# Kernel tuning notes

Measured on AMD Instinct MI355X. Metric: run time of the kernel, lower is better.

The kernel has to match this reference:

```python
import jax, jax.numpy as jnp
import numpy as np
import math

NH, DH, BS, LOCAL, RAND, NCLS = 12, 64, 49, 3, 3, 1
WINDOW = (8, 14, 14)
NKV = LOCAL + RAND


def make_rel_pos_index():
    ws = WINDOW
    rel_size = [2 * w - 1 for w in ws]
    coords = np.stack(np.meshgrid(*[np.arange(w) for w in ws], indexing='ij')).reshape(len(ws), -1)
    rel = (coords[:, :, None] - coords[:, None, :]).transpose(1, 2, 0).astype(np.int64)
    for i, w in enumerate(ws):
        rel[:, :, i] += w - 1
    for i, r in enumerate(rel_size[1:]):
        rel[:, :, :i + 1] *= r
    n = coords.shape[1]
    S = n + NCLS
    idx = np.zeros((S, S), dtype=np.int64)
    idx[NCLS:, NCLS:] = rel.sum(-1)
    start = int(np.prod(rel_size))
    idx[:NCLS, NCLS:] = np.arange(NCLS)[:, None] + start
    start += NCLS
    idx[NCLS:, :NCLS] = np.arange(NCLS)[None, :] + start
    start += NCLS
    idx[:NCLS, :NCLS] = np.arange(NCLS ** 2).reshape(NCLS, NCLS) + start
    return idx.astype(np.int32)


def setup_inputs() -> dict:
    key = jax.random.key(0)
    ks = jax.random.split(key, 8)
    B, S, D = 8, 1569, 768
    M = (S - NCLS) // BS  # 32 blocks
    hidden_states = jax.random.normal(ks[0], (B, S, D), dtype=jnp.float32)
    Wq = jax.random.normal(ks[1], (D, D), dtype=jnp.float32) * 0.02
    bq = jax.random.normal(ks[2], (D,), dtype=jnp.float32) * 0.02
    Wk = jax.random.normal(ks[3], (D, D), dtype=jnp.float32) * 0.02
    Wv = jax.random.normal(ks[4], (D, D), dtype=jnp.float32) * 0.02
    bv = jax.random.normal(ks[5], (D,), dtype=jnp.float32) * 0.02
    rel_table = jax.random.normal(ks[6], (10938, NH), dtype=jnp.float32) * 0.02
    rel_pos_index = jnp.asarray(make_rel_pos_index())
    rand_idx = jnp.sort(jax.random.randint(ks[7], (M, RAND), 0, M), axis=1).astype(jnp.int32)
    return {"hidden_states": hidden_states, "Wq": Wq, "bq": bq, "Wk": Wk, "Wv": Wv,
            "bv": bv, "rel_table": rel_table, "rel_pos_index": rel_pos_index, "rand_idx": rand_idx}


def reference(hidden_states, Wq, bq, Wk, Wv, bv, rel_table, rel_pos_index, rand_idx):
    B, S, D = hidden_states.shape
    scale = 1.0 / math.sqrt(DH)
    q = hidden_states @ Wq + bq
    k = hidden_states @ Wk          # key has no bias in BeitSelfAttention
    v = hidden_states @ Wv + bv
    split = lambda x: x.reshape(B, S, NH, DH).transpose(0, 2, 1, 3)  # b h s d
    q, k, v = split(q), split(k), split(v)

    # --- dense attention for cls queries over all keys ---
    cls_q = q[:, :, :NCLS]
    sim_cls = jnp.einsum('bhid,bhjd->bhij', cls_q, k) * scale
    bias_cls = rel_table[rel_pos_index[:NCLS, :]]           # [ncls, S, H]
    sim_cls = sim_cls + bias_cls.transpose(2, 0, 1)[None]
    attn_cls = jax.nn.softmax(sim_cls, axis=-1)
    out_cls = jnp.einsum('bhij,bhjd->bhid', attn_cls, v)    # [B,H,ncls,DH]

    # --- block-sparse attention for local queries ---
    loc_q = q[:, :, NCLS:]
    cls_k, loc_k = k[:, :, :NCLS], k[:, :, NCLS:]
    cls_v, loc_v = v[:, :, :NCLS], v[:, :, NCLS:]
    N = S - NCLS
    M = N // BS  # evenly divisible -> pad_q = 0
    qb = loc_q.reshape(B, NH, M, BS, DH)
    kb = loc_k.reshape(B, NH, M, BS, DH)
    vb = loc_v.reshape(B, NH, M, BS, DH)

    # local + random key-block indices per query block: [M, NKV]
    offs = jnp.arange(-(LOCAL // 2), LOCAL // 2 + 1)
    local_idx = (jnp.arange(M)[:, None] + offs[None, :]) % M
    attn_idx = jnp.concatenate([local_idx.astype(jnp.int32), rand_idx], axis=1)

    kg = kb[:, :, attn_idx]   # [B,H,M,NKV,BS,DH]
    vg = vb[:, :, attn_idx]

    sim_loc = jnp.einsum('bhmid,bhmnjd->bhminj', qb, kg).reshape(B, NH, M, BS, NKV * BS)
    sim_c = jnp.einsum('bhmid,bhjd->bhmij', qb, cls_k)       # [B,H,M,BS,ncls]
    sim = jnp.concatenate([sim_c, sim_loc], axis=-1) * scale

    # gathered relative-position bias: query tokens are ncls..S-1 in order
    key_tok = (NCLS + attn_idx[:, :, None] * BS + jnp.arange(BS)[None, None, :]).reshape(M, NKV * BS)
    to_idx = jnp.concatenate([jnp.broadcast_to(jnp.arange(NCLS)[None], (M, NCLS)), key_tok], axis=1)
    q_rows = rel_pos_index[NCLS:].reshape(M, BS, S)
    bias_idx = jnp.take_along_axis(q_rows, jnp.broadcast_to(to_idx[:, None, :], (M, BS, to_idx.shape[1])), axis=-1)
    bias = rel_table[bias_idx]                                # [M,BS,ncls+NKV*BS,H]
    sim = sim + bias.transpose(3, 0, 1, 2)[None]

    attn = jax.nn.softmax(sim, axis=-1)
    a_cls = attn[..., :NCLS]
    a_loc = attn[..., NCLS:].reshape(B, NH, M, BS, NKV, BS)
    out_loc = jnp.einsum('bhminj,bhmnjd->bhmid', a_loc, vg) \
            + jnp.einsum('bhmic,bhcd->bhmid', a_cls, cls_v)
    out_loc = out_loc.reshape(B, NH, N, DH)

    out = jnp.concatenate([out_cls, out_loc], axis=2)         # [B,H,S,DH]
    return out.transpose(0, 2, 1, 3).reshape(B, S, D)
```

## Files before the change

### kernel.cpp

```cpp
#include <hip/hip_runtime.h>


#define S_TOT   1569
#define NBATCH  8

__global__ __launch_bounds__(256) void gemm_f32(const float* __restrict__ hs,
                                                const float* __restrict__ Wq,
                                                const float* __restrict__ Wk,
                                                const float* __restrict__ Wv,
                                                const float* __restrict__ bq,
                                                const float* __restrict__ bv,
                                                float* __restrict__ Q,
                                                float* __restrict__ K,
                                                float* __restrict__ V,
                                                int b0, int nTok) {
    __shared__ float As[128][20];
    __shared__ float Bs[16][136];
    int tid = threadIdx.x;
    int t0 = blockIdx.x * 128;
    int n0 = blockIdx.y * 128;
    int which = n0 / 768;
    int ng0 = n0 - which * 768;
    const float* W = (which == 0) ? Wq : (which == 1 ? Wk : Wv);
    const float* Xb = hs + (size_t)b0 * S_TOT * 768;

    int tr = tid >> 4;
    int tc = tid & 15;

    int sat = tid >> 2;
    int sac4 = (tid & 3) * 4;
    int sbk = tid >> 4;
    int sbn = (tid & 15) * 8;

    int scg = ((tid & 3) ^ ((sat >> 3) & 3)) * 4;
    int rswz = (tr & 3);

    int ta0 = t0 + sat;       if (ta0 >= nTok) ta0 = nTok - 1;
    int ta1 = t0 + sat + 64;  if (ta1 >= nTok) ta1 = nTok - 1;

    float acc[8][8];
#pragma unroll
    for (int i = 0; i < 8; i++)
#pragma unroll
        for (int j = 0; j < 8; j++) acc[i][j] = 0.f;

    float4 pa0, pa1, pb0, pb1;
    {
        pa0 = *(const float4*)(Xb + (size_t)ta0 * 768 + 0 + sac4);
        pa1 = *(const float4*)(Xb + (size_t)ta1 * 768 + 0 + sac4);
        const float* wr_ = W + (size_t)(0 + sbk) * 768 + ng0 + sbn;
        pb0 = *(const float4*)(wr_);
        pb1 = *(const float4*)(wr_ + 4);
    }

    for (int k0 = 0; k0 < 768; k0 += 16) {
        *(float4*)&As[sat][scg]      = pa0;
        *(float4*)&As[sat + 64][scg] = pa1;
        *(float4*)&Bs[sbk][sbn]      = pb0;
        *(float4*)&Bs[sbk][sbn + 4]  = pb1;
        __syncthreads();

        if (k0 + 16 < 768) {
            int kn = k0 + 16;
            pa0 = *(const float4*)(Xb + (size_t)ta0 * 768 + kn + sac4);
            pa1 = *(const float4*)(Xb + (size_t)ta1 * 768 + kn + sac4);
            const float* wr_ = W + (size_t)(kn + sbk) * 768 + ng0 + sbn;
            pb0 = *(const float4*)(wr_);
            pb1 = *(const float4*)(wr_ + 4);
        }

#pragma unroll
        for (int kq = 0; kq < 4; kq++) {
            float4 xa[8];
            int rc = (kq ^ rswz) * 4;
#pragma unroll
            for (int i = 0; i < 8; i++)
                xa[i] = *(const float4*)&As[tr * 8 + i][rc];
#pragma unroll
            for (int kk = 0; kk < 4; kk++) {
                int k = kq * 4 + kk;
                float4 w0 = *(const float4*)&Bs[k][tc * 4];
                float4 w1 = *(const float4*)&Bs[k][64 + tc * 4];
#pragma unroll
                for (int i = 0; i < 8; i++) {
                    float a = (kk == 0) ? xa[i].x : (kk == 1) ? xa[i].y
                            : (kk == 2) ? xa[i].z : xa[i].w;
                    acc[i][0] = fmaf(a, w0.x, acc[i][0]);
                    acc[i][1] = fmaf(a, w0.y, acc[i][1]);
                    acc[i][2] = fmaf(a, w0.z, acc[i][2]);
                    acc[i][3] = fmaf(a, w0.w, acc[i][3]);
                    acc[i][4] = fmaf(a, w1.x, acc[i][4]);
                    acc[i][5] = fmaf(a, w1.y, acc[i][5]);
                    acc[i][6] = fmaf(a, w1.z, acc[i][6]);
                    acc[i][7] = fmaf(a, w1.w, acc[i][7]);
                }
            }
        }
        __syncthreads();
    }

    float* dst = (which == 0) ? Q : (which == 1 ? K : V);
    const float* bias = (which == 0) ? bq : (which == 2 ? bv : nullptr);
#pragma unroll
    for (int hh = 0; hh < 2; hh++) {
        int nn = ng0 + hh * 64 + tc * 4;
        int h = nn >> 6, d = nn & 63;
        float4 bv4 = make_float4(0.f, 0.f, 0.f, 0.f);
        if (bias) bv4 = *(const float4*)(bias + nn);
#pragma unroll
        for (int i = 0; i < 8; i++) {
            int t = t0 + tr * 8 + i;
            if (t >= nTok) continue;
            int bl = t / S_TOT;
            int s = t - bl * S_TOT;
            float4 o;
            o.x = acc[i][hh * 4 + 0] + bv4.x;
            o.y = acc[i][hh * 4 + 1] + bv4.y;
            o.z = acc[i][hh * 4 + 2] + bv4.z;
            o.w = acc[i][hh * 4 + 3] + bv4.w;
            *(float4*)(dst + ((size_t)(bl * 12 + h) * S_TOT + s) * 64 + d) = o;
        }
    }
}

__global__ __launch_bounds__(256) void cls_attn(const float* __restrict__ Q,
                                                const float* __restrict__ K,
                                                const float* __restrict__ V,
                                                const float* __restrict__ rel,
                                                const int* __restrict__ rpi,
                                                float* __restrict__ out, int b0) {
    int bh = blockIdx.x;
    int bl = bh / 12, h = bh - bl * 12;
    __shared__ float p[S_TOT];
    __shared__ float4 qs4[16];
    __shared__ float red[256];
    __shared__ float wred[8];
    int tid = threadIdx.x, lane = tid & 63, w = tid >> 6;
    size_t base = (size_t)bh * S_TOT * 64;
    const float* Qb = Q + base;
    const float* Kb = K + base;
    const float* Vb = V + base;
    if (tid < 64) ((float*)qs4)[tid] = Qb[tid];
    __syncthreads();

    float lmx = -1e30f;
    for (int j = tid; j < S_TOT; j += 256) {
        const float4* kr = (const float4*)(Kb + j * 64);
        float a = 0.f;
#pragma unroll
        for (int d4 = 0; d4 < 16; d4++) {
            float4 kv = kr[d4];
            float4 qv = qs4[d4];
            a = fmaf(qv.x, kv.x, a); a = fmaf(qv.y, kv.y, a);
            a = fmaf(qv.z, kv.z, a); a = fmaf(qv.w, kv.w, a);
        }
        a = a * 0.125f + rel[rpi[j] * 12 + h];
        p[j] = a;
        lmx = fmaxf(lmx, a);
    }
#pragma unroll
    for (int off = 32; off > 0; off >>= 1) lmx = fmaxf(lmx, __shfl_xor(lmx, off));
    if (lane == 0) wred[w] = lmx;
    __syncthreads();
    float mx = fmaxf(fmaxf(wred[0], wred[1]), fmaxf(wred[2], wred[3]));
    float lsum = 0.f;
    for (int j = tid; j < S_TOT; j += 256) {
        float e = __expf(p[j] - mx);
        p[j] = e;
        lsum += e;
    }
#pragma unroll
    for (int off = 32; off > 0; off >>= 1) lsum += __shfl_xor(lsum, off);
    if (lane == 0) wred[4 + w] = lsum;
    __syncthreads();
    float inv = 1.0f / (wred[4] + wred[5] + wred[6] + wred[7]);
    float acc = 0.f;
    for (int j = w; j < S_TOT; j += 4) acc = fmaf(p[j], Vb[j * 64 + lane], acc);
    red[w * 64 + lane] = acc;
    __syncthreads();
    if (w == 0) {
        float o = (red[lane] + red[64 + lane] + red[128 + lane] + red[192 + lane]) * inv;
        out[(size_t)(b0 + bl) * S_TOT * 768 + h * 64 + lane] = o;
    }
}

__global__ __launch_bounds__(256, 4) void loc_attn(const float* __restrict__ Q,
                                                   const float* __restrict__ K,
                                                   const float* __restrict__ V,
                                                   const float* __restrict__ rel,
                                                   const int* __restrict__ rand_idx,
                                                   float* __restrict__ out,
                                                   int b0, int ng) {
    int d = blockIdx.x;
    int xcd = d & 7, kk_ = d >> 3;
    int slot = xcd * (ng << 2) + kk_;
    int g = slot >> 5;
    int m = slot & 31;
    int h = g % 12;
    int bl = g / 12;

    __shared__ float Qlds[49][64];
    __shared__ float Plds[4][13][64];
    __shared__ unsigned short tok[320];
    int tid = threadIdx.x, lane = tid & 63, w = tid >> 6;

    size_t base = (size_t)((bl * 12 + h) * S_TOT) * 64;
    const float* Qb = Q + base;
    const float* Kb = K + base;
    const float* Vb = V + base;

    for (int jj = tid; jj < 320; jj += 256) {
        int t = 0;
        if (jj >= 1 && jj < 295) {
            int j1 = jj - 1;
            int n = j1 / 49;
            int q = j1 - n * 49;
            int a;
            if (n == 0)      a = (m + 31) & 31;
            else if (n == 1) a = m;
            else if (n == 2) a = (m + 1) & 31;
            else             a = rand_idx[m * 3 + (n - 3)];
            t = 1 + a * 49 + q;
        }
        tok[jj] = (unsigned short)t;
    }
    for (int idx = tid; idx < 49 * 64; idx += 256) {
        int r = idx >> 6, c = idx & 63;
        ((float*)Qlds)[idx] = Qb[(size_t)(1 + m * 49 + r) * 64 + c];
    }
    __syncthreads();

    int cq[13];
#pragma unroll
    for (int r = 0; r < 13; r++) {
        int i = w + 4 * r;
        int qr = 1 + m * 49 + i;
        if (qr > S_TOT - 1) qr = S_TOT - 1;
        int pq = qr - 1;
        int zq = pq / 196;
        int rem = pq - zq * 196;
        int yq = rem / 14;
        int xq = rem - yq * 14;
        cq[r] = zq * 729 + yq * 27 + xq;
    }

    float fl[13], facc[13];
#pragma unroll
    for (int r = 0; r < 13; r++) { fl[r] = 0.f; facc[r] = 0.f; }

    for (int jc = 0; jc < 5; jc++) {
        int j = jc * 64 + lane;
        int tj = tok[j];
        const float* kp = Kb + (size_t)tj * 64;

        int pj = tj - 1;
        int zj = pj / 196;
        int remj = pj - zj * 196;
        int yj = remj / 14;
        int xj = remj - yj * 14;
        int cj = zj * 729 + yj * 27 + xj;
        bool iscls = (tj == 0);

        float s[13];
#pragma unroll
        for (int r = 0; r < 13; r++) s[r] = 0.f;
#pragma unroll 4
        for (int d4 = 0; d4 < 16; d4++) {
            float4 kv = *(const float4*)(kp + d4 * 4);
#pragma unroll
            for (int r = 0; r < 13; r++) {
                int qrow = w + 4 * r;
                if (qrow > 48) qrow = 48;
                float4 qv = *(const float4*)&Qlds[qrow][d4 * 4];
                s[r] = fmaf(qv.x, kv.x, s[r]);
                s[r] = fmaf(qv.y, kv.y, s[r]);
                s[r] = fmaf(qv.z, kv.z, s[r]);
                s[r] = fmaf(qv.w, kv.w, s[r]);
            }
        }

        bool jv = j < 295;
#pragma unroll
        for (int r = 0; r < 13; r++) {
            int bidx = iscls ? 10936 : (cq[r] - cj + 5467);
            float e = jv ? __expf(fmaf(s[r], 0.125f, rel[bidx * 12 + h])) : 0.f;
            float ps = e;
#pragma unroll
            for (int off = 32; off > 0; off >>= 1) ps += __shfl_xor(ps, off);
            fl[r] += ps;
            Plds[w][r][lane] = e;
        }

#pragma unroll 4
        for (int jg = 0; jg < 16; jg++) {
            int jb = jc * 64 + jg * 4;
            int t0 = tok[jb + 0], t1 = tok[jb + 1], t2 = tok[jb + 2], t3 = tok[jb + 3];
            float v0 = Vb[(size_t)t0 * 64 + lane];
            float v1 = Vb[(size_t)t1 * 64 + lane];
            float v2 = Vb[(size_t)t2 * 64 + lane];
            float v3 = Vb[(size_t)t3 * 64 + lane];
#pragma unroll
            for (int r = 0; r < 13; r++) {
                float4 p4 = *(const float4*)&Plds[w][r][jg * 4];
                facc[r] = fmaf(p4.x, v0, facc[r]);
                facc[r] = fmaf(p4.y, v1, facc[r]);
                facc[r] = fmaf(p4.z, v2, facc[r]);
                facc[r] = fmaf(p4.w, v3, facc[r]);
            }
        }
    }

    int nrows = (w == 0) ? 13 : 12;
    for (int r = 0; r < nrows; r++) {
        int i = w + 4 * r;
        int st = 1 + m * 49 + i;
        out[((size_t)(b0 + bl) * S_TOT + st) * 768 + h * 64 + lane] = facc[r] / fl[r];
    }
}

extern "C" void kernel_launch(void* const* d_in, const int* in_sizes, int n_in,
                              void* d_out, int out_size, void* d_ws, size_t ws_size,
                              hipStream_t stream) {
    (void)in_sizes; (void)n_in; (void)out_size;
    const float* hs  = (const float*)d_in[0];
    const float* Wq  = (const float*)d_in[1];
    const float* bq  = (const float*)d_in[2];
    const float* Wk  = (const float*)d_in[3];
    const float* Wv  = (const float*)d_in[4];
    const float* bv  = (const float*)d_in[5];
    const float* rel = (const float*)d_in[6];
    const int*   rpi = (const int*)d_in[7];
    const int*   rnd = (const int*)d_in[8];
    float* out = (float*)d_out;
    char* ws = (char*)d_ws;

    constexpr size_t PBUF = (size_t)12 * S_TOT * 64 * 4;

    int C = 1;
    if (ws_size >= 3 * PBUF) {
        size_t c = ws_size / (3 * PBUF);
        C = (c >= NBATCH) ? NBATCH : (int)c;
        if (C < 1) C = 1;
    }
    float* Q = (float*)(ws);
    float* K = (float*)(ws + (size_t)C * PBUF);
    float* V = (float*)(ws + (size_t)C * PBUF * 2);

    for (int b0 = 0; b0 < NBATCH; b0 += C) {
        int cb = (NBATCH - b0 < C) ? (NBATCH - b0) : C;
        int nTok = cb * S_TOT;
        gemm_f32<<<dim3((nTok + 127) / 128, 18), dim3(256), 0, stream>>>(
            hs, Wq, Wk, Wv, bq, bv, Q, K, V, b0, nTok);
        cls_attn<<<dim3(12 * cb), dim3(256), 0, stream>>>(Q, K, V, rel, rpi, out, b0);
        int ngrp = 12 * cb;
        loc_attn<<<dim3(32 * ngrp), dim3(256), 0, stream>>>(
            Q, K, V, rel, rnd, out, b0, ngrp);
    }
}
```

Baseline: 1.162 ms.

## Double-buffer GEMM shared tiles and cut register pressure in local attention

The QKV GEMM now uses two shared-memory buffers for its A and B tiles. The next tile is written to the alternate buffer after compute, which removes one barrier per k-step. The local attention kernel splits the 13-row score computation into two halves of 7 and 6 rows. It also moves the per-row query coordinates and softmax partial sums from registers into shared memory, aiming to lower VGPR use so that the 4-blocks-per-CU launch bound holds without spilling. The cost is twice the GEMM's LDS footprint, which may reduce its occupancy, plus extra LDS traffic in the attention kernel.

Measured after the change: 1.126 ms. 3.1% less time.

```diff
diff --git a/kernel.cpp b/kernel.cpp
--- a/kernel.cpp
+++ b/kernel.cpp
@@ -14,8 +14,8 @@
                                                 float* __restrict__ K,
                                                 float* __restrict__ V,
                                                 int b0, int nTok) {
-    __shared__ float As[128][20];
-    __shared__ float Bs[16][136];
+    __shared__ float As[2][128][20];
+    __shared__ float Bs[2][16][136];
     int tid = threadIdx.x;
     int t0 = blockIdx.x * 128;
     int n0 = blockIdx.y * 128;
@@ -52,15 +52,16 @@
         pb0 = *(const float4*)(wr_);
         pb1 = *(const float4*)(wr_ + 4);
     }
-
+    *(float4*)&As[0][sat][scg]      = pa0;
+    *(float4*)&As[0][sat + 64][scg] = pa1;
+    *(float4*)&Bs[0][sbk][sbn]      = pb0;
+    *(float4*)&Bs[0][sbk][sbn + 4]  = pb1;
+    __syncthreads();
+
+    int cur = 0;
     for (int k0 = 0; k0 < 768; k0 += 16) {
-        *(float4*)&As[sat][scg]      = pa0;
-        *(float4*)&As[sat + 64][scg] = pa1;
-        *(float4*)&Bs[sbk][sbn]      = pb0;
-        *(float4*)&Bs[sbk][sbn + 4]  = pb1;
-        __syncthreads();
-
-        if (k0 + 16 < 768) {
+        bool has_next = (k0 + 16 < 768);
+        if (has_next) {
             int kn = k0 + 16;
             pa0 = *(const float4*)(Xb + (size_t)ta0 * 768 + kn + sac4);
             pa1 = *(const float4*)(Xb + (size_t)ta1 * 768 + kn + sac4);
@@ -75,12 +76,12 @@
             int rc = (kq ^ rswz) * 4;
 #pragma unroll
             for (int i = 0; i < 8; i++)
-                xa[i] = *(const float4*)&As[tr * 8 + i][rc];
+                xa[i] = *(const float4*)&As[cur][tr * 8 + i][rc];
 #pragma unroll
             for (int kk = 0; kk < 4; kk++) {
                 int k = kq * 4 + kk;
-                float4 w0 = *(const float4*)&Bs[k][tc * 4];
-                float4 w1 = *(const float4*)&Bs[k][64 + tc * 4];
+                float4 w0 = *(const float4*)&Bs[cur][k][tc * 4];
+                float4 w1 = *(const float4*)&Bs[cur][k][64 + tc * 4];
 #pragma unroll
                 for (int i = 0; i < 8; i++) {
                     float a = (kk == 0) ? xa[i].x : (kk == 1) ? xa[i].y
@@ -96,7 +97,16 @@
                 }
             }
         }
-        __syncthreads();
+
+        if (has_next) {
+            int nxt = cur ^ 1;
+            *(float4*)&As[nxt][sat][scg]      = pa0;
+            *(float4*)&As[nxt][sat + 64][scg] = pa1;
+            *(float4*)&Bs[nxt][sbk][sbn]      = pb0;
+            *(float4*)&Bs[nxt][sbk][sbn + 4]  = pb1;
+            __syncthreads();
+            cur = nxt;
+        }
     }
 
     float* dst = (which == 0) ? Q : (which == 1 ? K : V);
@@ -201,6 +211,8 @@
 
     __shared__ float Qlds[49][64];
     __shared__ float Plds[4][13][64];
+    __shared__ float flds[4][13][5];
+    __shared__ int   cqlds[52];
     __shared__ unsigned short tok[320];
     int tid = threadIdx.x, lane = tid & 63, w = tid >> 6;
 
@@ -224,29 +236,25 @@
         }
         tok[jj] = (unsigned short)t;
     }
-    for (int idx = tid; idx < 49 * 64; idx += 256) {
-        int r = idx >> 6, c = idx & 63;
-        ((float*)Qlds)[idx] = Qb[(size_t)(1 + m * 49 + r) * 64 + c];
-    }
-    __syncthreads();
-
-    int cq[13];
-#pragma unroll
-    for (int r = 0; r < 13; r++) {
-        int i = w + 4 * r;
-        int qr = 1 + m * 49 + i;
+    if (tid < 52) {
+        int qr = 1 + m * 49 + tid;
         if (qr > S_TOT - 1) qr = S_TOT - 1;
         int pq = qr - 1;
         int zq = pq / 196;
         int rem = pq - zq * 196;
         int yq = rem / 14;
         int xq = rem - yq * 14;
-        cq[r] = zq * 729 + yq * 27 + xq;
-    }
-
-    float fl[13], facc[13];
-#pragma unroll
-    for (int r = 0; r < 13; r++) { fl[r] = 0.f; facc[r] = 0.f; }
+        cqlds[tid] = zq * 729 + yq * 27 + xq;
+    }
+    for (int idx = tid; idx < 49 * 64; idx += 256) {
+        int r = idx >> 6, c = idx & 63;
+        ((float*)Qlds)[idx] = Qb[(size_t)(1 + m * 49 + r) * 64 + c];
+    }
+    __syncthreads();
+
+    float facc[13];
+#pragma unroll
+    for (int r = 0; r < 13; r++) facc[r] = 0.f;
 
     for (int jc = 0; jc < 5; jc++) {
         int j = jc * 64 + lane;
@@ -258,37 +266,44 @@
         int remj = pj - zj * 196;
         int yj = remj / 14;
         int xj = remj - yj * 14;
-        int cj = zj * 729 + yj * 27 + xj;
+        int cjb = 5467 - (zj * 729 + yj * 27 + xj);
         bool iscls = (tj == 0);
-
-        float s[13];
-#pragma unroll
-        for (int r = 0; r < 13; r++) s[r] = 0.f;
+        bool jv = j < 295;
+
+#pragma unroll
+        for (int half = 0; half < 2; half++) {
+            const int r0 = half * 7;
+            const int RN = half ? 6 : 7;
+            float s[7];
+#pragma unroll
+            for (int rr = 0; rr < 7; rr++) s[rr] = 0.f;
 #pragma unroll 4
-        for (int d4 = 0; d4 < 16; d4++) {
-            float4 kv = *(const float4*)(kp + d4 * 4);
-#pragma unroll
-            for (int r = 0; r < 13; r++) {
-                int qrow = w + 4 * r;
-                if (qrow > 48) qrow = 48;
-                float4 qv = *(const float4*)&Qlds[qrow][d4 * 4];
-                s[r] = fmaf(qv.x, kv.x, s[r]);
-                s[r] = fmaf(qv.y, kv.y, s[r]);
-                s[r] = fmaf(qv.z, kv.z, s[r]);
-                s[r] = fmaf(qv.w, kv.w, s[r]);
+            for (int d4 = 0; d4 < 16; d4++) {
+                float4 kv = *(const float4*)(kp + d4 * 4);
+#pragma unroll
+                for (int rr = 0; rr < RN; rr++) {
+                    int qrow = w + 4 * (r0 + rr);
+                    if (qrow > 48) qrow = 48;
+                    float4 qv = *(const float4*)&Qlds[qrow][d4 * 4];
+                    s[rr] = fmaf(qv.x, kv.x, s[rr]);
+                    s[rr] = fmaf(qv.y, kv.y, s[rr]);
+                    s[rr] = fmaf(qv.z, kv.z, s[rr]);
+                    s[rr] = fmaf(qv.w, kv.w, s[rr]);
+                }
             }
-        }
-
-        bool jv = j < 295;
-#pragma unroll
-        for (int r = 0; r < 13; r++) {
-            int bidx = iscls ? 10936 : (cq[r] - cj + 5467);
-            float e = jv ? __expf(fmaf(s[r], 0.125f, rel[bidx * 12 + h])) : 0.f;
-            float ps = e;
-#pragma unroll
-            for (int off = 32; off > 0; off >>= 1) ps += __shfl_xor(ps, off);
-            fl[r] += ps;
-            Plds[w][r][lane] = e;
+#pragma unroll
+            for (int rr = 0; rr < RN; rr++) {
+                int r = r0 + rr;
+                int i = w + 4 * r;
+                int ii = (i > 48) ? 48 : i;
+                int bidx = iscls ? 10936 : (cqlds[ii] + cjb);
+                float e = jv ? __expf(fmaf(s[rr], 0.125f, rel[bidx * 12 + h])) : 0.f;
+                float ps = e;
+#pragma unroll
+                for (int off = 32; off > 0; off >>= 1) ps += __shfl_xor(ps, off);
+                if (lane == 0) flds[w][r][jc] = ps;
+                Plds[w][r][lane] = e;
+            }
         }
 
 #pragma unroll 4
@@ -312,9 +327,11 @@
 
     int nrows = (w == 0) ? 13 : 12;
     for (int r = 0; r < nrows; r++) {
+        float fl = ((flds[w][r][0] + flds[w][r][1]) + (flds[w][r][2] + flds[w][r][3]))
+                 + flds[w][r][4];
         int i = w + 4 * r;
         int st = 1 + m * 49 + i;
-        out[((size_t)(b0 + bl) * S_TOT + st) * 768 + h * 64 + lane] = facc[r] / fl[r];
+        out[((size_t)(b0 + bl) * S_TOT + st) * 768 + h * 64 + lane] = facc[r] / fl;
     }
 }
 
```
